# Kernel optimization log

Measured on AMD Instinct MI355X. Metric: run time of the kernel, lower is better.

Reference implementation:

```python
import jax, jax.numpy as jnp
import numpy as np

BS, NINP, NHID, K, T = 2048, 512, 512, 16, 8
M = NHID // K  # per-block hidden = 32
ATT_D = 16     # read/write key dim
TAU = 0.5


def setup_inputs() -> dict:
    key = jax.random.key(0)
    ks = jax.random.split(key, 10)
    s = 0.1
    return {
        "x": jax.random.normal(ks[0], (BS, NINP), jnp.float32),
        "h": jax.random.normal(ks[1], (BS, NHID), jnp.float32),
        # stacked GRUCell params across templates (torch gate order: r, z, n)
        "W_ih": jax.random.normal(ks[2], (T, 3 * M, NINP), jnp.float32) * s,
        "W_hh": jax.random.normal(ks[3], (T, 3 * M, M), jnp.float32) * s,
        "b_ih": jax.random.normal(ks[4], (T, 3 * M), jnp.float32) * s,
        "b_hh": jax.random.normal(ks[5], (T, 3 * M), jnp.float32) * s,
        # GroupLinearLayer weights (no bias): read has 1 group, write has T groups
        "w_read": jax.random.normal(ks[6], (1, M, ATT_D), jnp.float32) * s,
        "w_write": jax.random.normal(ks[7], (T, M, ATT_D), jnp.float32) * s,
        # pre-sampled Gumbel noise for gumbel_softmax, shape [bs*k, T]
        "gumbel_noise": jax.random.gumbel(ks[8], (BS * K, T), jnp.float32),
    }


def reference(x, h, W_ih, W_hh, b_ih, b_hh, w_read, w_write, gumbel_noise):
    bs = h.shape[0]
    N = bs * K
    # blockify hidden: [bs, nhid] -> [N, m]
    h2 = h.reshape(N, M)
    # tile input across blocks: [bs, ninp] -> [N, ninp]
    xin = jnp.broadcast_to(x[:, None, :], (bs, K, NINP)).reshape(N, NINP)
    # read key: GroupLinearLayer with 1 group -> [N, ATT_D]
    h_read = h2 @ w_read[0]
    # all-template GRUCell as two grouped GEMMs: [T, N, 3m]
    gi = jnp.einsum('ni,tgi->tng', xin, W_ih) + b_ih[:, None, :]
    gh = jnp.einsum('nm,tgm->tng', h2, W_hh) + b_hh[:, None, :]
    r = jax.nn.sigmoid(gi[..., :M] + gh[..., :M])
    z = jax.nn.sigmoid(gi[..., M:2 * M] + gh[..., M:2 * M])
    n = jnp.tanh(gi[..., 2 * M:] + r * gh[..., 2 * M:])
    hnext = (1.0 - z) * n + z * h2[None]            # [T, N, m]
    hnext = hnext.transpose(1, 0, 2)                # [N, T, m]
    # write keys: grouped linear per template -> [N, T, ATT_D]
    write_key = jnp.einsum('ntm,tmf->ntf', hnext, w_write)
    # attention logits: bmm(h_read[N,1,f], write_key^T) -> [N, T]
    logits = jnp.einsum('nf,ntf->nt', h_read, write_key)
    # hard gumbel-softmax (tau=0.5) with straight-through estimator
    y_soft = jax.nn.softmax((logits + gumbel_noise) / TAU, axis=-1)
    y_hard = jax.nn.one_hot(jnp.argmax(y_soft, axis=-1), T, dtype=y_soft.dtype)
    att = y_hard + y_soft - jax.lax.stop_gradient(y_soft)  # [N, T]
    # combine templates (bmm with [N,1,T] then mean over singleton dim)
    h_out = jnp.einsum('nt,ntm->nm', att, hnext)    # [N, m]
    h_out = h_out.reshape(bs, K * M)
    att_out = jax.lax.stop_gradient(att).reshape(bs, K, T)
    return h_out, att_out
```

## Files before the change

### kernel.cpp

```cpp
#include <hip/hip_runtime.h>

#define NB_BS   2048
#define NB_NINP 512
#define NB_NHID 512
#define NB_K    16
#define NB_T    8
#define NB_M    32
#define NB_C    768
#define H_OUT_ELEMS (NB_BS * NB_NHID)

__global__ __launch_bounds__(256, 2)
void k1_gemm_gi(const float* __restrict__ x, const float* __restrict__ Wih,
                const float* __restrict__ bih, const float* __restrict__ bhh,
                float* __restrict__ gi)
{
    __shared__ __align__(16) float As[32][34];
    __shared__ __align__(16) float Bs[32][100];

    const int tid  = threadIdx.x;
    const int row0 = blockIdx.x * 32;
    const int col0 = blockIdx.y * 96;
    const int wave = tid >> 6, lane = tid & 63;
    const int rg   = lane >> 2;
    const int cg   = lane & 3;
    const int wc0  = wave * 24 + cg * 6;

    const int arow = tid >> 3, akq = (tid & 7) * 4;
    const int c0 = tid >> 3,          kq0 = (tid & 7) * 4;
    const int c1 = (tid + 256) >> 3,  kq1 = ((tid + 256) & 7) * 4;
    const int c2 = (tid + 512) >> 3,  kq2 = ((tid + 512) & 7) * 4;

    const float* xp = x + (size_t)(row0 + arow) * NB_NINP + akq;
    float4 a0 = *(const float4*)xp;
    float4 b0 = *(const float4*)&Wih[(size_t)(col0 + c0) * NB_NINP + kq0];
    float4 b1 = *(const float4*)&Wih[(size_t)(col0 + c1) * NB_NINP + kq1];
    float4 b2 = *(const float4*)&Wih[(size_t)(col0 + c2) * NB_NINP + kq2];

    float acc[2][6];
    #pragma unroll
    for (int i = 0; i < 2; ++i)
        #pragma unroll
        for (int e = 0; e < 6; ++e) acc[i][e] = 0.f;

    for (int kb = 0; kb < NB_NINP; kb += 32) {
        __syncthreads();
        As[akq+0][arow]=a0.x; As[akq+1][arow]=a0.y;
        As[akq+2][arow]=a0.z; As[akq+3][arow]=a0.w;
        Bs[kq0+0][c0]=b0.x; Bs[kq0+1][c0]=b0.y; Bs[kq0+2][c0]=b0.z; Bs[kq0+3][c0]=b0.w;
        Bs[kq1+0][c1]=b1.x; Bs[kq1+1][c1]=b1.y; Bs[kq1+2][c1]=b1.z; Bs[kq1+3][c1]=b1.w;
        Bs[kq2+0][c2]=b2.x; Bs[kq2+1][c2]=b2.y; Bs[kq2+2][c2]=b2.z; Bs[kq2+3][c2]=b2.w;
        __syncthreads();
        if (kb + 32 < NB_NINP) {
            a0 = *(const float4*)(xp + kb + 32);
            b0 = *(const float4*)&Wih[(size_t)(col0 + c0) * NB_NINP + kb + 32 + kq0];
            b1 = *(const float4*)&Wih[(size_t)(col0 + c1) * NB_NINP + kb + 32 + kq1];
            b2 = *(const float4*)&Wih[(size_t)(col0 + c2) * NB_NINP + kb + 32 + kq2];
        }
        #pragma unroll
        for (int kk = 0; kk < 32; ++kk) {
            const float2 av = *(const float2*)&As[kk][rg * 2];
            const float2 w0 = *(const float2*)&Bs[kk][wc0];
            const float2 w1 = *(const float2*)&Bs[kk][wc0 + 2];
            const float2 w2 = *(const float2*)&Bs[kk][wc0 + 4];
            const float avv[2] = {av.x, av.y};
            const float wvv[6] = {w0.x, w0.y, w1.x, w1.y, w2.x, w2.y};
            #pragma unroll
            for (int i = 0; i < 2; ++i)
                #pragma unroll
                for (int e = 0; e < 6; ++e)
                    acc[i][e] = fmaf(avv[i], wvv[e], acc[i][e]);
        }
    }

    float bias[6];
    #pragma unroll
    for (int e = 0; e < 6; ++e) {
        const int cl = wc0 + e;
        const int c  = col0 + cl;
        bias[e] = bih[c] + (cl < 64 ? bhh[c] : 0.f);
    }
    #pragma unroll
    for (int i = 0; i < 2; ++i) {
        const size_t base = (size_t)(row0 + rg * 2 + i) * NB_C + col0 + wc0;
        #pragma unroll
        for (int e = 0; e < 6; e += 2) {
            float2 o; o.x = acc[i][e] + bias[e]; o.y = acc[i][e+1] + bias[e+1];
            *(float2*)&gi[base + e] = o;
        }
    }
}

__global__ __launch_bounds__(1024)
__attribute__((amdgpu_waves_per_eu(4, 4)))
void k2_fused(const float* __restrict__ h,      const float* __restrict__ Whh,
              const float* __restrict__ bhh,    const float* __restrict__ wread,
              const float* __restrict__ wwrite, const float* __restrict__ gumb,
              const float* __restrict__ gi,     float* __restrict__ out)
{
    __shared__ __align__(16) float4 P[3][32][64];
    __shared__ float WWT[NB_T * 16 * 32];
    __shared__ __align__(16) float WR[512];
    __shared__ __align__(16) float HT[8][32][20];
    __shared__ __align__(16) float HR2T[8][16][20];

    const int tid  = threadIdx.x;
    const int wave = tid >> 6, lane = tid & 63;
    const int bl   = wave >> 1, kh = wave & 1;
    const int b    = blockIdx.x * 8 + bl;
    const int m_   = lane & 31, half = lane >> 5;

    float* PF = (float*)P;
    for (int i = tid; i < 24576; i += 1024) {
        const int c = i >> 5, mm = i & 31;
        const int t = c / 96, rem = c - t * 96;
        const int gc = rem >> 5, mout = rem & 31;
        const int j  = (t >> 1) * 3 + gc;
        const int sl = ((t & 1) * 32 + mout) ^ (mm & 7);
        PF[(((j >> 2) * 32 + mm) * 64 + sl) * 4 + (j & 3)] = Whh[i];
    }
    for (int i = tid; i < 4096; i += 1024) {
        const int t = i >> 9, mo = (i >> 4) & 31, f = i & 15;
        WWT[t * 512 + f * 32 + mo] = wwrite[i];
    }
    if (tid < 512) WR[tid] = wread[tid];
    #pragma unroll
    for (int e = 0; e < 4; ++e) {
        const int idx = kh * 256 + e * 64 + lane;
        HT[bl][idx & 31][idx >> 5] = h[(size_t)b * NB_NHID + idx];
    }
    __syncthreads();

    {
        const int kq = kh * 8 + (lane >> 3);
        const int f0 = (lane & 7) * 2;
        float s0 = 0.f, s1 = 0.f;
        #pragma unroll 8
        for (int mm = 0; mm < 32; ++mm) {
            const float hv = HT[bl][mm][kq];
            s0 = fmaf(hv, WR[mm * 16 + f0], s0);
            s1 = fmaf(hv, WR[mm * 16 + f0 + 1], s1);
        }
        HR2T[bl][f0    ][kq] = s0;
        HR2T[bl][f0 + 1][kq] = s1;
    }

    float gi_r[4][3], bhn[4];
    #pragma unroll
    for (int p = 0; p < 4; ++p) {
        const int t = 2 * p + half;
        #pragma unroll
        for (int gc = 0; gc < 3; ++gc)
            gi_r[p][gc] = gi[(size_t)b * NB_C + t * 96 + gc * 32 + m_];
        bhn[p] = bhh[t * 96 + 64 + m_];
    }

    #pragma unroll 1
    for (int pass = 0; pass < 2; ++pass) {
        const int k0 = kh * 8 + pass * 4;

        float acc[4][12];
        #pragma unroll
        for (int r = 0; r < 4; ++r)
            #pragma unroll
            for (int j = 0; j < 12; ++j) acc[r][j] = 0.f;

        #pragma unroll 4
        for (int mm = 0; mm < 32; ++mm) {
            const int sw = lane ^ (mm & 7);
            const float4 w0 = P[0][mm][sw];
            const float4 w1 = P[1][mm][sw];
            const float4 w2 = P[2][mm][sw];
            const float4 hv = *(const float4*)&HT[bl][mm][k0];
            const float wj[12] = {w0.x,w0.y,w0.z,w0.w, w1.x,w1.y,w1.z,w1.w,
                                  w2.x,w2.y,w2.z,w2.w};
            const float hr4[4] = {hv.x, hv.y, hv.z, hv.w};
            #pragma unroll
            for (int r = 0; r < 4; ++r)
                #pragma unroll
                for (int j = 0; j < 12; ++j)
                    acc[r][j] = fmaf(hr4[r], wj[j], acc[r][j]);
        }

        float ww[4][4];
        #pragma unroll
        for (int r = 0; r < 4; ++r)
            #pragma unroll
            for (int p = 0; p < 4; ++p) ww[r][p] = 0.f;
        #pragma unroll 4
        for (int f = 0; f < 16; ++f) {
            float wt[4];
            #pragma unroll
            for (int p = 0; p < 4; ++p)
                wt[p] = WWT[(2 * p + half) * 512 + f * 32 + m_];
            const float4 hka = *(const float4*)&HR2T[bl][f][k0];
            const float hk[4] = {hka.x, hka.y, hka.z, hka.w};
            #pragma unroll
            for (int r = 0; r < 4; ++r)
                #pragma unroll
                for (int p = 0; p < 4; ++p)
                    ww[r][p] = fmaf(hk[r], wt[p], ww[r][p]);
        }

        #pragma unroll
        for (int r = 0; r < 4; ++r) {
            const int k = k0 + r;
            const float h2v = HT[bl][m_][k];
            float hn[4], lg[4];
            #pragma unroll
            for (int p = 0; p < 4; ++p) {
                const float xr = gi_r[p][0] + acc[r][p*3+0];
                const float xz = gi_r[p][1] + acc[r][p*3+1];
                const float gn = bhn[p]     + acc[r][p*3+2];
                const float rg = 1.f / (1.f + __expf(-xr));
                const float zg = 1.f / (1.f + __expf(-xz));
                const float xn = gi_r[p][2] + rg * gn;
                const float e2 = __expf(2.f * xn);
                const float tn = 1.f - 2.f / (e2 + 1.f);
                const float hv2 = (1.f - zg) * tn + zg * h2v;
                hn[p] = hv2;
                float part = hv2 * ww[r][p];
                part += __shfl_xor(part, 1, 64);
                part += __shfl_xor(part, 2, 64);
                part += __shfl_xor(part, 4, 64);
                part += __shfl_xor(part, 8, 64);
                part += __shfl_xor(part, 16, 64);
                lg[p] = part;
            }
            float s[8];
            #pragma unroll
            for (int p = 0; p < 4; ++p) {
                const float oth = __shfl_xor(lg[p], 32, 64);
                s[2*p]   = half ? oth   : lg[p];
                s[2*p+1] = half ? lg[p] : oth;
            }
            const float* gp = gumb + ((size_t)b * NB_K + k) * NB_T;
            const float4 ga = *(const float4*)gp;
            const float4 gb = *(const float4*)(gp + 4);
            const float gv[8] = {ga.x,ga.y,ga.z,ga.w, gb.x,gb.y,gb.z,gb.w};
            float best = s[0] + gv[0]; int bt = 0;
            #pragma unroll
            for (int t2 = 1; t2 < 8; ++t2) {
                const float v = s[t2] + gv[t2];
                if (v > best) { best = v; bt = t2; }
            }
            const int pstar = bt >> 1, hstar = bt & 1;
            float hsel = hn[0];
            hsel = (pstar == 1) ? hn[1] : hsel;
            hsel = (pstar == 2) ? hn[2] : hsel;
            hsel = (pstar == 3) ? hn[3] : hsel;
            if (half == hstar)
                out[(size_t)b * NB_NHID + k * 32 + m_] = hsel;
            if (lane < 8)
                out[H_OUT_ELEMS + ((size_t)b * NB_K + k) * NB_T + lane] =
                    (lane == bt) ? 1.f : 0.f;
        }
    }
}

extern "C" void kernel_launch(void* const* d_in, const int* in_sizes, int n_in,
                              void* d_out, int out_size, void* d_ws, size_t ws_size,
                              hipStream_t stream) {
    const float* x      = (const float*)d_in[0];
    const float* h      = (const float*)d_in[1];
    const float* Wih    = (const float*)d_in[2];
    const float* Whh    = (const float*)d_in[3];
    const float* bih    = (const float*)d_in[4];
    const float* bhh    = (const float*)d_in[5];
    const float* wread  = (const float*)d_in[6];
    const float* wwrite = (const float*)d_in[7];
    const float* gumb   = (const float*)d_in[8];
    float* out = (float*)d_out;
    float* gi  = (float*)d_ws;

    k1_gemm_gi<<<dim3(64, 8), 256, 0, stream>>>(x, Wih, bih, bhh, gi);
    k2_fused<<<dim3(256), 1024, 0, stream>>>(h, Whh, bhh, wread, wwrite,
                                             gumb, gi, out);
}
```

Measured before the change: 96.34 us.

## Retile gi GEMM to 64-wide columns and split GRU templates across wave pairs

The input GEMM now uses 32x64 output tiles with a K-step of 64, which gives 768 blocks instead of 512 and lets it use float4 LDS reads and stores. The fused GRU kernel now has each wave pair split the 8 templates rather than the 16 blocks. Each wave computes all 16 blocks for its 4 templates, and the logits are exchanged through shared memory before the argmax. This aims to cut redundant h loads and shuffle work and to improve load balance, at the cost of a larger accumulator array (96 floats) that raises register pressure.

```diff
diff --git a/kernel.cpp b/kernel.cpp
--- a/kernel.cpp
+++ b/kernel.cpp
@@ -9,84 +9,87 @@
 #define NB_C    768
 #define H_OUT_ELEMS (NB_BS * NB_NHID)
 
-__global__ __launch_bounds__(256, 2)
+__global__ __launch_bounds__(256, 3)
 void k1_gemm_gi(const float* __restrict__ x, const float* __restrict__ Wih,
                 const float* __restrict__ bih, const float* __restrict__ bhh,
                 float* __restrict__ gi)
 {
-    __shared__ __align__(16) float As[32][34];
-    __shared__ __align__(16) float Bs[32][100];
+    __shared__ __align__(16) float As[64][34];
+    __shared__ __align__(16) float Bs[64][68];
 
     const int tid  = threadIdx.x;
     const int row0 = blockIdx.x * 32;
-    const int col0 = blockIdx.y * 96;
+    const int col0 = blockIdx.y * 64;
     const int wave = tid >> 6, lane = tid & 63;
     const int rg   = lane >> 2;
     const int cg   = lane & 3;
-    const int wc0  = wave * 24 + cg * 6;
-
-    const int arow = tid >> 3, akq = (tid & 7) * 4;
-    const int c0 = tid >> 3,          kq0 = (tid & 7) * 4;
-    const int c1 = (tid + 256) >> 3,  kq1 = ((tid + 256) & 7) * 4;
-    const int c2 = (tid + 512) >> 3,  kq2 = ((tid + 512) & 7) * 4;
-
-    const float* xp = x + (size_t)(row0 + arow) * NB_NINP + akq;
-    float4 a0 = *(const float4*)xp;
-    float4 b0 = *(const float4*)&Wih[(size_t)(col0 + c0) * NB_NINP + kq0];
-    float4 b1 = *(const float4*)&Wih[(size_t)(col0 + c1) * NB_NINP + kq1];
-    float4 b2 = *(const float4*)&Wih[(size_t)(col0 + c2) * NB_NINP + kq2];
-
-    float acc[2][6];
+    const int wc0  = wave * 16 + cg * 4;
+
+    const int ar0 = tid >> 4,           ak0 = (tid & 15) * 4;
+    const int ar1 = (tid + 256) >> 4,   ak1 = ((tid + 256) & 15) * 4;
+    int bc[4], bk[4];
+    #pragma unroll
+    for (int l = 0; l < 4; ++l) {
+        const int q = l * 256 + tid;
+        bc[l] = q >> 4; bk[l] = (q & 15) * 4;
+    }
+
+    float4 a0 = *(const float4*)&x[(size_t)(row0 + ar0) * NB_NINP + ak0];
+    float4 a1 = *(const float4*)&x[(size_t)(row0 + ar1) * NB_NINP + ak1];
+    float4 bfr[4];
+    #pragma unroll
+    for (int l = 0; l < 4; ++l)
+        bfr[l] = *(const float4*)&Wih[(size_t)(col0 + bc[l]) * NB_NINP + bk[l]];
+
+    float acc[2][4];
     #pragma unroll
     for (int i = 0; i < 2; ++i)
         #pragma unroll
-        for (int e = 0; e < 6; ++e) acc[i][e] = 0.f;
-
-    for (int kb = 0; kb < NB_NINP; kb += 32) {
+        for (int e = 0; e < 4; ++e) acc[i][e] = 0.f;
+
+    for (int kb = 0; kb < NB_NINP; kb += 64) {
         __syncthreads();
-        As[akq+0][arow]=a0.x; As[akq+1][arow]=a0.y;
-        As[akq+2][arow]=a0.z; As[akq+3][arow]=a0.w;
-        Bs[kq0+0][c0]=b0.x; Bs[kq0+1][c0]=b0.y; Bs[kq0+2][c0]=b0.z; Bs[kq0+3][c0]=b0.w;
-        Bs[kq1+0][c1]=b1.x; Bs[kq1+1][c1]=b1.y; Bs[kq1+2][c1]=b1.z; Bs[kq1+3][c1]=b1.w;
-        Bs[kq2+0][c2]=b2.x; Bs[kq2+1][c2]=b2.y; Bs[kq2+2][c2]=b2.z; Bs[kq2+3][c2]=b2.w;
+        As[ak0+0][ar0]=a0.x; As[ak0+1][ar0]=a0.y; As[ak0+2][ar0]=a0.z; As[ak0+3][ar0]=a0.w;
+        As[ak1+0][ar1]=a1.x; As[ak1+1][ar1]=a1.y; As[ak1+2][ar1]=a1.z; As[ak1+3][ar1]=a1.w;
+        #pragma unroll
+        for (int l = 0; l < 4; ++l) {
+            Bs[bk[l]+0][bc[l]]=bfr[l].x; Bs[bk[l]+1][bc[l]]=bfr[l].y;
+            Bs[bk[l]+2][bc[l]]=bfr[l].z; Bs[bk[l]+3][bc[l]]=bfr[l].w;
+        }
         __syncthreads();
-        if (kb + 32 < NB_NINP) {
-            a0 = *(const float4*)(xp + kb + 32);
-            b0 = *(const float4*)&Wih[(size_t)(col0 + c0) * NB_NINP + kb + 32 + kq0];
-            b1 = *(const float4*)&Wih[(size_t)(col0 + c1) * NB_NINP + kb + 32 + kq1];
-            b2 = *(const float4*)&Wih[(size_t)(col0 + c2) * NB_NINP + kb + 32 + kq2];
-        }
-        #pragma unroll
-        for (int kk = 0; kk < 32; ++kk) {
+        if (kb + 64 < NB_NINP) {
+            a0 = *(const float4*)&x[(size_t)(row0 + ar0) * NB_NINP + kb + 64 + ak0];
+            a1 = *(const float4*)&x[(size_t)(row0 + ar1) * NB_NINP + kb + 64 + ak1];
+            #pragma unroll
+            for (int l = 0; l < 4; ++l)
+                bfr[l] = *(const float4*)&Wih[(size_t)(col0 + bc[l]) * NB_NINP + kb + 64 + bk[l]];
+        }
+        #pragma unroll 16
+        for (int kk = 0; kk < 64; ++kk) {
             const float2 av = *(const float2*)&As[kk][rg * 2];
-            const float2 w0 = *(const float2*)&Bs[kk][wc0];
-            const float2 w1 = *(const float2*)&Bs[kk][wc0 + 2];
-            const float2 w2 = *(const float2*)&Bs[kk][wc0 + 4];
+            const float4 wv = *(const float4*)&Bs[kk][wc0];
             const float avv[2] = {av.x, av.y};
-            const float wvv[6] = {w0.x, w0.y, w1.x, w1.y, w2.x, w2.y};
+            const float wvv[4] = {wv.x, wv.y, wv.z, wv.w};
             #pragma unroll
             for (int i = 0; i < 2; ++i)
                 #pragma unroll
-                for (int e = 0; e < 6; ++e)
+                for (int e = 0; e < 4; ++e)
                     acc[i][e] = fmaf(avv[i], wvv[e], acc[i][e]);
         }
     }
 
-    float bias[6];
-    #pragma unroll
-    for (int e = 0; e < 6; ++e) {
-        const int cl = wc0 + e;
-        const int c  = col0 + cl;
-        bias[e] = bih[c] + (cl < 64 ? bhh[c] : 0.f);
+    float bias[4];
+    #pragma unroll
+    for (int e = 0; e < 4; ++e) {
+        const int c = col0 + wc0 + e;
+        bias[e] = bih[c] + ((c % 96) < 64 ? bhh[c] : 0.f);
     }
     #pragma unroll
     for (int i = 0; i < 2; ++i) {
-        const size_t base = (size_t)(row0 + rg * 2 + i) * NB_C + col0 + wc0;
-        #pragma unroll
-        for (int e = 0; e < 6; e += 2) {
-            float2 o; o.x = acc[i][e] + bias[e]; o.y = acc[i][e+1] + bias[e+1];
-            *(float2*)&gi[base + e] = o;
-        }
+        float4 o;
+        o.x = acc[i][0] + bias[0]; o.y = acc[i][1] + bias[1];
+        o.z = acc[i][2] + bias[2]; o.w = acc[i][3] + bias[3];
+        *(float4*)&gi[(size_t)(row0 + rg * 2 + i) * NB_C + col0 + wc0] = o;
     }
 }
 
@@ -97,41 +100,40 @@
               const float* __restrict__ wwrite, const float* __restrict__ gumb,
               const float* __restrict__ gi,     float* __restrict__ out)
 {
-    __shared__ __align__(16) float4 P[3][32][64];
-    __shared__ float WWT[NB_T * 16 * 32];
+    __shared__ __align__(16) float P2[2][3][32][128];
+    __shared__ __align__(16) float WWT2[2][16][128];
     __shared__ __align__(16) float WR[512];
     __shared__ __align__(16) float HT[8][32][20];
     __shared__ __align__(16) float HR2T[8][16][20];
+    __shared__ __align__(16) float LG[8][16][8];
 
     const int tid  = threadIdx.x;
     const int wave = tid >> 6, lane = tid & 63;
-    const int bl   = wave >> 1, kh = wave & 1;
+    const int bl   = wave >> 1, tq = wave & 1;
     const int b    = blockIdx.x * 8 + bl;
     const int m_   = lane & 31, half = lane >> 5;
 
-    float* PF = (float*)P;
     for (int i = tid; i < 24576; i += 1024) {
         const int c = i >> 5, mm = i & 31;
         const int t = c / 96, rem = c - t * 96;
         const int gc = rem >> 5, mout = rem & 31;
-        const int j  = (t >> 1) * 3 + gc;
-        const int sl = ((t & 1) * 32 + mout) ^ (mm & 7);
-        PF[(((j >> 2) * 32 + mm) * 64 + sl) * 4 + (j & 3)] = Whh[i];
+        const int slot = (((t >> 1) & 1) * 32 + mout) ^ mm;
+        P2[t >> 2][gc][mm][slot * 2 + (t & 1)] = Whh[i];
     }
     for (int i = tid; i < 4096; i += 1024) {
         const int t = i >> 9, mo = (i >> 4) & 31, f = i & 15;
-        WWT[t * 512 + f * 32 + mo] = wwrite[i];
+        WWT2[t >> 2][f][(((t >> 1) & 1) * 32 + mo) * 2 + (t & 1)] = wwrite[i];
     }
     if (tid < 512) WR[tid] = wread[tid];
     #pragma unroll
     for (int e = 0; e < 4; ++e) {
-        const int idx = kh * 256 + e * 64 + lane;
+        const int idx = tq * 256 + e * 64 + lane;
         HT[bl][idx & 31][idx >> 5] = h[(size_t)b * NB_NHID + idx];
     }
     __syncthreads();
 
     {
-        const int kq = kh * 8 + (lane >> 3);
+        const int kq = tq * 8 + (lane >> 3);
         const int f0 = (lane & 7) * 2;
         float s0 = 0.f, s1 = 0.f;
         #pragma unroll 8
@@ -144,116 +146,115 @@
         HR2T[bl][f0 + 1][kq] = s1;
     }
 
-    float gi_r[4][3], bhn[4];
-    #pragma unroll
-    for (int p = 0; p < 4; ++p) {
-        const int t = 2 * p + half;
+    float acc[16][6];
+    #pragma unroll
+    for (int k = 0; k < 16; ++k)
+        #pragma unroll
+        for (int j = 0; j < 6; ++j) acc[k][j] = 0.f;
+
+    #pragma unroll 1
+    for (int mm = 0; mm < 32; ++mm) {
+        const int sl2 = (lane ^ mm) * 2;
+        const float2 w0 = *(const float2*)&P2[tq][0][mm][sl2];
+        const float2 w1 = *(const float2*)&P2[tq][1][mm][sl2];
+        const float2 w2 = *(const float2*)&P2[tq][2][mm][sl2];
+        #pragma unroll
+        for (int q = 0; q < 4; ++q) {
+            const float4 hv = *(const float4*)&HT[bl][mm][q * 4];
+            const float hr[4] = {hv.x, hv.y, hv.z, hv.w};
+            #pragma unroll
+            for (int r = 0; r < 4; ++r) {
+                const int k = q * 4 + r;
+                acc[k][0] = fmaf(hr[r], w0.x, acc[k][0]);
+                acc[k][1] = fmaf(hr[r], w1.x, acc[k][1]);
+                acc[k][2] = fmaf(hr[r], w2.x, acc[k][2]);
+                acc[k][3] = fmaf(hr[r], w0.y, acc[k][3]);
+                acc[k][4] = fmaf(hr[r], w1.y, acc[k][4]);
+                acc[k][5] = fmaf(hr[r], w2.y, acc[k][5]);
+            }
+        }
+    }
+    __syncthreads();
+
+    float gi_r[2][3], bhn[2];
+    #pragma unroll
+    for (int u = 0; u < 2; ++u) {
+        const int t = tq * 4 + half * 2 + u;
         #pragma unroll
         for (int gc = 0; gc < 3; ++gc)
-            gi_r[p][gc] = gi[(size_t)b * NB_C + t * 96 + gc * 32 + m_];
-        bhn[p] = bhh[t * 96 + 64 + m_];
-    }
-
-    #pragma unroll 1
-    for (int pass = 0; pass < 2; ++pass) {
-        const int k0 = kh * 8 + pass * 4;
-
-        float acc[4][12];
-        #pragma unroll
-        for (int r = 0; r < 4; ++r)
-            #pragma unroll
-            for (int j = 0; j < 12; ++j) acc[r][j] = 0.f;
-
-        #pragma unroll 4
-        for (int mm = 0; mm < 32; ++mm) {
-            const int sw = lane ^ (mm & 7);
-            const float4 w0 = P[0][mm][sw];
-            const float4 w1 = P[1][mm][sw];
-            const float4 w2 = P[2][mm][sw];
-            const float4 hv = *(const float4*)&HT[bl][mm][k0];
-            const float wj[12] = {w0.x,w0.y,w0.z,w0.w, w1.x,w1.y,w1.z,w1.w,
-                                  w2.x,w2.y,w2.z,w2.w};
-            const float hr4[4] = {hv.x, hv.y, hv.z, hv.w};
-            #pragma unroll
-            for (int r = 0; r < 4; ++r)
-                #pragma unroll
-                for (int j = 0; j < 12; ++j)
-                    acc[r][j] = fmaf(hr4[r], wj[j], acc[r][j]);
-        }
-
-        float ww[4][4];
-        #pragma unroll
-        for (int r = 0; r < 4; ++r)
-            #pragma unroll
-            for (int p = 0; p < 4; ++p) ww[r][p] = 0.f;
+            gi_r[u][gc] = gi[(size_t)b * NB_C + t * 96 + gc * 32 + m_];
+        bhn[u] = bhh[t * 96 + 64 + m_];
+    }
+
+    float hn[16][2];
+    #pragma unroll
+    for (int q = 0; q < 4; ++q) {
+        float ww[4][2];
+        #pragma unroll
+        for (int r = 0; r < 4; ++r) { ww[r][0] = 0.f; ww[r][1] = 0.f; }
         #pragma unroll 4
         for (int f = 0; f < 16; ++f) {
-            float wt[4];
-            #pragma unroll
-            for (int p = 0; p < 4; ++p)
-                wt[p] = WWT[(2 * p + half) * 512 + f * 32 + m_];
-            const float4 hka = *(const float4*)&HR2T[bl][f][k0];
-            const float hk[4] = {hka.x, hka.y, hka.z, hka.w};
-            #pragma unroll
-            for (int r = 0; r < 4; ++r)
-                #pragma unroll
-                for (int p = 0; p < 4; ++p)
-                    ww[r][p] = fmaf(hk[r], wt[p], ww[r][p]);
-        }
-
+            const float2 wt = *(const float2*)&WWT2[tq][f][lane * 2];
+            const float4 hk = *(const float4*)&HR2T[bl][f][q * 4];
+            const float hh[4] = {hk.x, hk.y, hk.z, hk.w};
+            #pragma unroll
+            for (int r = 0; r < 4; ++r) {
+                ww[r][0] = fmaf(hh[r], wt.x, ww[r][0]);
+                ww[r][1] = fmaf(hh[r], wt.y, ww[r][1]);
+            }
+        }
         #pragma unroll
         for (int r = 0; r < 4; ++r) {
-            const int k = k0 + r;
+            const int k = q * 4 + r;
             const float h2v = HT[bl][m_][k];
-            float hn[4], lg[4];
-            #pragma unroll
-            for (int p = 0; p < 4; ++p) {
-                const float xr = gi_r[p][0] + acc[r][p*3+0];
-                const float xz = gi_r[p][1] + acc[r][p*3+1];
-                const float gn = bhn[p]     + acc[r][p*3+2];
+            float lg2[2];
+            #pragma unroll
+            for (int u = 0; u < 2; ++u) {
+                const float xr = gi_r[u][0] + acc[k][u*3+0];
+                const float xz = gi_r[u][1] + acc[k][u*3+1];
+                const float gn = bhn[u]     + acc[k][u*3+2];
                 const float rg = 1.f / (1.f + __expf(-xr));
                 const float zg = 1.f / (1.f + __expf(-xz));
-                const float xn = gi_r[p][2] + rg * gn;
+                const float xn = gi_r[u][2] + rg * gn;
                 const float e2 = __expf(2.f * xn);
                 const float tn = 1.f - 2.f / (e2 + 1.f);
                 const float hv2 = (1.f - zg) * tn + zg * h2v;
-                hn[p] = hv2;
-                float part = hv2 * ww[r][p];
+                hn[k][u] = hv2;
+                float part = hv2 * ww[r][u];
                 part += __shfl_xor(part, 1, 64);
                 part += __shfl_xor(part, 2, 64);
                 part += __shfl_xor(part, 4, 64);
                 part += __shfl_xor(part, 8, 64);
                 part += __shfl_xor(part, 16, 64);
-                lg[p] = part;
-            }
-            float s[8];
-            #pragma unroll
-            for (int p = 0; p < 4; ++p) {
-                const float oth = __shfl_xor(lg[p], 32, 64);
-                s[2*p]   = half ? oth   : lg[p];
-                s[2*p+1] = half ? lg[p] : oth;
-            }
-            const float* gp = gumb + ((size_t)b * NB_K + k) * NB_T;
-            const float4 ga = *(const float4*)gp;
-            const float4 gb = *(const float4*)(gp + 4);
-            const float gv[8] = {ga.x,ga.y,ga.z,ga.w, gb.x,gb.y,gb.z,gb.w};
-            float best = s[0] + gv[0]; int bt = 0;
-            #pragma unroll
-            for (int t2 = 1; t2 < 8; ++t2) {
-                const float v = s[t2] + gv[t2];
-                if (v > best) { best = v; bt = t2; }
-            }
-            const int pstar = bt >> 1, hstar = bt & 1;
-            float hsel = hn[0];
-            hsel = (pstar == 1) ? hn[1] : hsel;
-            hsel = (pstar == 2) ? hn[2] : hsel;
-            hsel = (pstar == 3) ? hn[3] : hsel;
-            if (half == hstar)
-                out[(size_t)b * NB_NHID + k * 32 + m_] = hsel;
-            if (lane < 8)
-                out[H_OUT_ELEMS + ((size_t)b * NB_K + k) * NB_T + lane] =
-                    (lane == bt) ? 1.f : 0.f;
-        }
+                lg2[u] = part;
+            }
+            if (m_ == 0) {
+                LG[bl][k][tq * 4 + half * 2 + 0] = lg2[0];
+                LG[bl][k][tq * 4 + half * 2 + 1] = lg2[1];
+            }
+        }
+    }
+    __syncthreads();
+
+    #pragma unroll
+    for (int k = 0; k < 16; ++k) {
+        const float4 l0 = *(const float4*)&LG[bl][k][0];
+        const float4 l1 = *(const float4*)&LG[bl][k][4];
+        const float* gp = gumb + ((size_t)b * NB_K + k) * NB_T;
+        const float4 g0 = *(const float4*)gp;
+        const float4 g1 = *(const float4*)(gp + 4);
+        const float s[8] = {l0.x+g0.x, l0.y+g0.y, l0.z+g0.z, l0.w+g0.w,
+                            l1.x+g1.x, l1.y+g1.y, l1.z+g1.z, l1.w+g1.w};
+        float best = s[0]; int bt = 0;
+        #pragma unroll
+        for (int t2 = 1; t2 < 8; ++t2)
+            if (s[t2] > best) { best = s[t2]; bt = t2; }
+        const float hsel = (bt & 1) ? hn[k][1] : hn[k][0];
+        if ((bt >> 2) == tq && ((bt >> 1) & 1) == half)
+            out[(size_t)b * NB_NHID + k * 32 + m_] = hsel;
+        if (tq == 0 && lane < 8)
+            out[H_OUT_ELEMS + ((size_t)b * NB_K + k) * NB_T + lane] =
+                (lane == bt) ? 1.f : 0.f;
     }
 }
 
@@ -272,7 +273,7 @@
     float* out = (float*)d_out;
     float* gi  = (float*)d_ws;
 
-    k1_gemm_gi<<<dim3(64, 8), 256, 0, stream>>>(x, Wih, bih, bhh, gi);
+    k1_gemm_gi<<<dim3(64, 12), 256, 0, stream>>>(x, Wih, bih, bhh, gi);
     k2_fused<<<dim3(256), 1024, 0, stream>>>(h, Whh, bhh, wread, wwrite,
                                              gumb, gi, out);
 }
```

Result: slower. 104.2 us (+8.2%).

## Restructure gi GEMM with split-K 1024-thread blocks and vectorize write-key loads

Applied to the files above, without the earlier changes.

The input-gate GEMM now uses 64x96 tiles in 1024-thread blocks. The K dimension is split in half across two 512-thread groups, and their partial sums are reduced through shared memory before bias is added and the result stored. The grid becomes 256 blocks, sized to fill the CU count, instead of 512 smaller blocks. Separately, the write-key weights in the fused kernel are laid out so each thread fetches its four template weights with one float4 LDS load instead of four scalar loads. In exchange there is an extra shared-memory reduction and sync, a larger LDS footprint, and scalar global stores instead of float2 stores.

```diff
diff --git a/kernel.cpp b/kernel.cpp
--- a/kernel.cpp
+++ b/kernel.cpp
@@ -9,83 +9,95 @@
 #define NB_C    768
 #define H_OUT_ELEMS (NB_BS * NB_NHID)
 
-__global__ __launch_bounds__(256, 2)
+__global__ __launch_bounds__(1024)
 void k1_gemm_gi(const float* __restrict__ x, const float* __restrict__ Wih,
                 const float* __restrict__ bih, const float* __restrict__ bhh,
                 float* __restrict__ gi)
 {
-    __shared__ __align__(16) float As[32][34];
-    __shared__ __align__(16) float Bs[32][100];
+    __shared__ __align__(16) float As[2][32][68];
+    __shared__ __align__(16) float Bs[2][32][100];
+    __shared__ float ACCX[512][13];
 
     const int tid  = threadIdx.x;
-    const int row0 = blockIdx.x * 32;
+    const int kg   = tid >> 9;
+    const int ttid = tid & 511;
+    const int row0 = blockIdx.x * 64;
     const int col0 = blockIdx.y * 96;
-    const int wave = tid >> 6, lane = tid & 63;
-    const int rg   = lane >> 2;
-    const int cg   = lane & 3;
-    const int wc0  = wave * 24 + cg * 6;
-
-    const int arow = tid >> 3, akq = (tid & 7) * 4;
-    const int c0 = tid >> 3,          kq0 = (tid & 7) * 4;
-    const int c1 = (tid + 256) >> 3,  kq1 = ((tid + 256) & 7) * 4;
-    const int c2 = (tid + 512) >> 3,  kq2 = ((tid + 512) & 7) * 4;
-
-    const float* xp = x + (size_t)(row0 + arow) * NB_NINP + akq;
-    float4 a0 = *(const float4*)xp;
-    float4 b0 = *(const float4*)&Wih[(size_t)(col0 + c0) * NB_NINP + kq0];
-    float4 b1 = *(const float4*)&Wih[(size_t)(col0 + c1) * NB_NINP + kq1];
-    float4 b2 = *(const float4*)&Wih[(size_t)(col0 + c2) * NB_NINP + kq2];
-
-    float acc[2][6];
+    const int rg   = ttid >> 5;
+    const int cg   = ttid & 31;
+    const int kb0  = kg * 256;
+
+    const int ar = ttid >> 3, akq = (ttid & 7) * 4;
+    const int bc0 = ttid >> 3,        bkq0 = (ttid & 7) * 4;
+    const int bc1 = 64 + (ttid >> 3), bkq1 = (ttid & 7) * 4;
+
+    float4 a0 = *(const float4*)&x[(size_t)(row0 + ar) * NB_NINP + kb0 + akq];
+    float4 b0 = *(const float4*)&Wih[(size_t)(col0 + bc0) * NB_NINP + kb0 + bkq0];
+    float4 b1;
+    if (ttid < 256)
+        b1 = *(const float4*)&Wih[(size_t)(col0 + bc1) * NB_NINP + kb0 + bkq1];
+
+    float acc[4][3];
     #pragma unroll
-    for (int i = 0; i < 2; ++i)
-        #pragma unroll
-        for (int e = 0; e < 6; ++e) acc[i][e] = 0.f;
-
-    for (int kb = 0; kb < NB_NINP; kb += 32) {
+    for (int i = 0; i < 4; ++i)
+        #pragma unroll
+        for (int e = 0; e < 3; ++e) acc[i][e] = 0.f;
+
+    for (int slab = 0; slab < 8; ++slab) {
         __syncthreads();
-        As[akq+0][arow]=a0.x; As[akq+1][arow]=a0.y;
-        As[akq+2][arow]=a0.z; As[akq+3][arow]=a0.w;
-        Bs[kq0+0][c0]=b0.x; Bs[kq0+1][c0]=b0.y; Bs[kq0+2][c0]=b0.z; Bs[kq0+3][c0]=b0.w;
-        Bs[kq1+0][c1]=b1.x; Bs[kq1+1][c1]=b1.y; Bs[kq1+2][c1]=b1.z; Bs[kq1+3][c1]=b1.w;
-        Bs[kq2+0][c2]=b2.x; Bs[kq2+1][c2]=b2.y; Bs[kq2+2][c2]=b2.z; Bs[kq2+3][c2]=b2.w;
+        As[kg][akq+0][ar]=a0.x; As[kg][akq+1][ar]=a0.y;
+        As[kg][akq+2][ar]=a0.z; As[kg][akq+3][ar]=a0.w;
+        Bs[kg][bkq0+0][bc0]=b0.x; Bs[kg][bkq0+1][bc0]=b0.y;
+        Bs[kg][bkq0+2][bc0]=b0.z; Bs[kg][bkq0+3][bc0]=b0.w;
+        if (ttid < 256) {
+            Bs[kg][bkq1+0][bc1]=b1.x; Bs[kg][bkq1+1][bc1]=b1.y;
+            Bs[kg][bkq1+2][bc1]=b1.z; Bs[kg][bkq1+3][bc1]=b1.w;
+        }
         __syncthreads();
-        if (kb + 32 < NB_NINP) {
-            a0 = *(const float4*)(xp + kb + 32);
-            b0 = *(const float4*)&Wih[(size_t)(col0 + c0) * NB_NINP + kb + 32 + kq0];
-            b1 = *(const float4*)&Wih[(size_t)(col0 + c1) * NB_NINP + kb + 32 + kq1];
-            b2 = *(const float4*)&Wih[(size_t)(col0 + c2) * NB_NINP + kb + 32 + kq2];
+        if (slab < 7) {
+            const int kb = kb0 + (slab + 1) * 32;
+            a0 = *(const float4*)&x[(size_t)(row0 + ar) * NB_NINP + kb + akq];
+            b0 = *(const float4*)&Wih[(size_t)(col0 + bc0) * NB_NINP + kb + bkq0];
+            if (ttid < 256)
+                b1 = *(const float4*)&Wih[(size_t)(col0 + bc1) * NB_NINP + kb + bkq1];
         }
         #pragma unroll
         for (int kk = 0; kk < 32; ++kk) {
-            const float2 av = *(const float2*)&As[kk][rg * 2];
-            const float2 w0 = *(const float2*)&Bs[kk][wc0];
-            const float2 w1 = *(const float2*)&Bs[kk][wc0 + 2];
-            const float2 w2 = *(const float2*)&Bs[kk][wc0 + 4];
-            const float avv[2] = {av.x, av.y};
-            const float wvv[6] = {w0.x, w0.y, w1.x, w1.y, w2.x, w2.y};
-            #pragma unroll
-            for (int i = 0; i < 2; ++i)
-                #pragma unroll
-                for (int e = 0; e < 6; ++e)
-                    acc[i][e] = fmaf(avv[i], wvv[e], acc[i][e]);
-        }
-    }
-
-    float bias[6];
-    #pragma unroll
-    for (int e = 0; e < 6; ++e) {
-        const int cl = wc0 + e;
-        const int c  = col0 + cl;
-        bias[e] = bih[c] + (cl < 64 ? bhh[c] : 0.f);
-    }
-    #pragma unroll
-    for (int i = 0; i < 2; ++i) {
-        const size_t base = (size_t)(row0 + rg * 2 + i) * NB_C + col0 + wc0;
-        #pragma unroll
-        for (int e = 0; e < 6; e += 2) {
-            float2 o; o.x = acc[i][e] + bias[e]; o.y = acc[i][e+1] + bias[e+1];
-            *(float2*)&gi[base + e] = o;
+            const float4 av = *(const float4*)&As[kg][kk][rg * 4];
+            const float w0 = Bs[kg][kk][cg];
+            const float w1 = Bs[kg][kk][cg + 32];
+            const float w2 = Bs[kg][kk][cg + 64];
+            const float avv[4] = {av.x, av.y, av.z, av.w};
+            #pragma unroll
+            for (int i = 0; i < 4; ++i) {
+                acc[i][0] = fmaf(avv[i], w0, acc[i][0]);
+                acc[i][1] = fmaf(avv[i], w1, acc[i][1]);
+                acc[i][2] = fmaf(avv[i], w2, acc[i][2]);
+            }
+        }
+    }
+
+    __syncthreads();
+    if (kg == 1) {
+        #pragma unroll
+        for (int i = 0; i < 4; ++i)
+            #pragma unroll
+            for (int e = 0; e < 3; ++e) ACCX[ttid][i * 3 + e] = acc[i][e];
+    }
+    __syncthreads();
+    if (kg == 0) {
+        float bias[3];
+        #pragma unroll
+        for (int e = 0; e < 3; ++e) {
+            const int c = col0 + cg + e * 32;
+            bias[e] = bih[c] + (e < 2 ? bhh[c] : 0.f);
+        }
+        #pragma unroll
+        for (int i = 0; i < 4; ++i) {
+            const size_t base = (size_t)(row0 + rg * 4 + i) * NB_C + col0 + cg;
+            #pragma unroll
+            for (int e = 0; e < 3; ++e)
+                gi[base + e * 32] = acc[i][e] + ACCX[ttid][i * 3 + e] + bias[e];
         }
     }
 }
@@ -98,7 +110,7 @@
               const float* __restrict__ gi,     float* __restrict__ out)
 {
     __shared__ __align__(16) float4 P[3][32][64];
-    __shared__ float WWT[NB_T * 16 * 32];
+    __shared__ __align__(16) float4 WWT4[16][64];
     __shared__ __align__(16) float WR[512];
     __shared__ __align__(16) float HT[8][32][20];
     __shared__ __align__(16) float HR2T[8][16][20];
@@ -120,7 +132,7 @@
     }
     for (int i = tid; i < 4096; i += 1024) {
         const int t = i >> 9, mo = (i >> 4) & 31, f = i & 15;
-        WWT[t * 512 + f * 32 + mo] = wwrite[i];
+        ((float*)WWT4)[(f * 64 + (t & 1) * 32 + mo) * 4 + (t >> 1)] = wwrite[i];
     }
     if (tid < 512) WR[tid] = wread[tid];
     #pragma unroll
@@ -188,11 +200,9 @@
             for (int p = 0; p < 4; ++p) ww[r][p] = 0.f;
         #pragma unroll 4
         for (int f = 0; f < 16; ++f) {
-            float wt[4];
-            #pragma unroll
-            for (int p = 0; p < 4; ++p)
-                wt[p] = WWT[(2 * p + half) * 512 + f * 32 + m_];
+            const float4 wt4 = WWT4[f][half * 32 + m_];
             const float4 hka = *(const float4*)&HR2T[bl][f][k0];
+            const float wt[4] = {wt4.x, wt4.y, wt4.z, wt4.w};
             const float hk[4] = {hka.x, hka.y, hka.z, hka.w};
             #pragma unroll
             for (int r = 0; r < 4; ++r)
@@ -272,7 +282,7 @@
     float* out = (float*)d_out;
     float* gi  = (float*)d_ws;
 
-    k1_gemm_gi<<<dim3(64, 8), 256, 0, stream>>>(x, Wih, bih, bhh, gi);
+    k1_gemm_gi<<<dim3(32, 8), 1024, 0, stream>>>(x, Wih, bih, bhh, gi);
     k2_fused<<<dim3(256), 1024, 0, stream>>>(h, Whh, bhh, wread, wwrite,
                                              gumb, gi, out);
 }
```

After: 87.47 us. 1.1x faster.

## Retile gi GEMM with double-buffered LDS and vectorize write-key reductions

Applied to the files above, without the earlier changes.

The input-gate GEMM is retiled to 64-column, 64-deep k-tiles. It double-buffers shared memory, which removes one barrier per step, and XOR-swizzles the B tile so float4 reads avoid bank conflicts. The grid grows to 64x12 blocks with a higher occupancy hint. In the fused kernel, write-key weights are repacked so each lane loads one float4 per step instead of four scalars. The per-template logit reduction now shares butterfly shuffles across templates and gathers the eight logits through a small LDS array instead of extra cross-half shuffles. The risks are higher register and LDS use in the GEMM and a same-wave LDS exchange that relies on ordering within the wave.

```diff
diff --git a/kernel.cpp b/kernel.cpp
--- a/kernel.cpp
+++ b/kernel.cpp
@@ -9,84 +9,113 @@
 #define NB_C    768
 #define H_OUT_ELEMS (NB_BS * NB_NHID)
 
-__global__ __launch_bounds__(256, 2)
+__global__ __launch_bounds__(256, 3)
 void k1_gemm_gi(const float* __restrict__ x, const float* __restrict__ Wih,
                 const float* __restrict__ bih, const float* __restrict__ bhh,
                 float* __restrict__ gi)
 {
-    __shared__ __align__(16) float As[32][34];
-    __shared__ __align__(16) float Bs[32][100];
+    __shared__ __align__(16) float As[2][64][34];
+    __shared__ __align__(16) float Bs[2][64][68];
 
     const int tid  = threadIdx.x;
     const int row0 = blockIdx.x * 32;
-    const int col0 = blockIdx.y * 96;
-    const int wave = tid >> 6, lane = tid & 63;
-    const int rg   = lane >> 2;
-    const int cg   = lane & 3;
-    const int wc0  = wave * 24 + cg * 6;
-
-    const int arow = tid >> 3, akq = (tid & 7) * 4;
-    const int c0 = tid >> 3,          kq0 = (tid & 7) * 4;
-    const int c1 = (tid + 256) >> 3,  kq1 = ((tid + 256) & 7) * 4;
-    const int c2 = (tid + 512) >> 3,  kq2 = ((tid + 512) & 7) * 4;
-
-    const float* xp = x + (size_t)(row0 + arow) * NB_NINP + akq;
-    float4 a0 = *(const float4*)xp;
-    float4 b0 = *(const float4*)&Wih[(size_t)(col0 + c0) * NB_NINP + kq0];
-    float4 b1 = *(const float4*)&Wih[(size_t)(col0 + c1) * NB_NINP + kq1];
-    float4 b2 = *(const float4*)&Wih[(size_t)(col0 + c2) * NB_NINP + kq2];
-
-    float acc[2][6];
+    const int col0 = blockIdx.y * 64;
+    const int rg   = tid & 15;
+    const int cg   = tid >> 4;
+
+    const int akq  = (tid & 15) * 4;
+    const int ar0  = tid >> 4, ar1 = ar0 + 16;
+    const int swz  = (tid & 7) * 4;
+
+    const float* xb = x   + (size_t)row0 * NB_NINP + akq;
+    const float* wb = Wih + (size_t)col0 * NB_NINP + akq;
+
+    float4 a0 = *(const float4*)&xb[(size_t)ar0 * NB_NINP];
+    float4 a1 = *(const float4*)&xb[(size_t)ar1 * NB_NINP];
+    float4 bf[4];
+    #pragma unroll
+    for (int L = 0; L < 4; ++L)
+        bf[L] = *(const float4*)&wb[(size_t)(L * 16 + (tid >> 4)) * NB_NINP];
+
+    float acc[2][4];
     #pragma unroll
     for (int i = 0; i < 2; ++i)
         #pragma unroll
-        for (int e = 0; e < 6; ++e) acc[i][e] = 0.f;
-
-    for (int kb = 0; kb < NB_NINP; kb += 32) {
-        __syncthreads();
-        As[akq+0][arow]=a0.x; As[akq+1][arow]=a0.y;
-        As[akq+2][arow]=a0.z; As[akq+3][arow]=a0.w;
-        Bs[kq0+0][c0]=b0.x; Bs[kq0+1][c0]=b0.y; Bs[kq0+2][c0]=b0.z; Bs[kq0+3][c0]=b0.w;
-        Bs[kq1+0][c1]=b1.x; Bs[kq1+1][c1]=b1.y; Bs[kq1+2][c1]=b1.z; Bs[kq1+3][c1]=b1.w;
-        Bs[kq2+0][c2]=b2.x; Bs[kq2+1][c2]=b2.y; Bs[kq2+2][c2]=b2.z; Bs[kq2+3][c2]=b2.w;
-        __syncthreads();
-        if (kb + 32 < NB_NINP) {
-            a0 = *(const float4*)(xp + kb + 32);
-            b0 = *(const float4*)&Wih[(size_t)(col0 + c0) * NB_NINP + kb + 32 + kq0];
-            b1 = *(const float4*)&Wih[(size_t)(col0 + c1) * NB_NINP + kb + 32 + kq1];
-            b2 = *(const float4*)&Wih[(size_t)(col0 + c2) * NB_NINP + kb + 32 + kq2];
-        }
-        #pragma unroll
-        for (int kk = 0; kk < 32; ++kk) {
-            const float2 av = *(const float2*)&As[kk][rg * 2];
-            const float2 w0 = *(const float2*)&Bs[kk][wc0];
-            const float2 w1 = *(const float2*)&Bs[kk][wc0 + 2];
-            const float2 w2 = *(const float2*)&Bs[kk][wc0 + 4];
+        for (int e = 0; e < 4; ++e) acc[i][e] = 0.f;
+
+    {
+        const float av0[4] = {a0.x, a0.y, a0.z, a0.w};
+        const float av1[4] = {a1.x, a1.y, a1.z, a1.w};
+        #pragma unroll
+        for (int j = 0; j < 4; ++j) {
+            As[0][akq + j][ar0] = av0[j];
+            As[0][akq + j][ar1] = av1[j];
+        }
+        #pragma unroll
+        for (int L = 0; L < 4; ++L) {
+            const float bv[4] = {bf[L].x, bf[L].y, bf[L].z, bf[L].w};
+            const int bcol = (L * 16 + (tid >> 4)) ^ swz;
+            #pragma unroll
+            for (int j = 0; j < 4; ++j) Bs[0][akq + j][bcol] = bv[j];
+        }
+    }
+    __syncthreads();
+
+    for (int s = 0; s < 8; ++s) {
+        const int buf = s & 1;
+        if (s < 7) {
+            const int kb = (s + 1) * 64;
+            a0 = *(const float4*)&xb[(size_t)ar0 * NB_NINP + kb];
+            a1 = *(const float4*)&xb[(size_t)ar1 * NB_NINP + kb];
+            #pragma unroll
+            for (int L = 0; L < 4; ++L)
+                bf[L] = *(const float4*)&wb[(size_t)(L * 16 + (tid >> 4)) * NB_NINP + kb];
+        }
+        #pragma unroll 16
+        for (int kk = 0; kk < 64; ++kk) {
+            const int sB = ((kk >> 2) & 7) * 4;
+            const float2 av = *(const float2*)&As[buf][kk][rg * 2];
+            const float4 wv = *(const float4*)&Bs[buf][kk][(cg * 4) ^ sB];
             const float avv[2] = {av.x, av.y};
-            const float wvv[6] = {w0.x, w0.y, w1.x, w1.y, w2.x, w2.y};
+            const float wvv[4] = {wv.x, wv.y, wv.z, wv.w};
             #pragma unroll
             for (int i = 0; i < 2; ++i)
                 #pragma unroll
-                for (int e = 0; e < 6; ++e)
+                for (int e = 0; e < 4; ++e)
                     acc[i][e] = fmaf(avv[i], wvv[e], acc[i][e]);
         }
-    }
-
-    float bias[6];
-    #pragma unroll
-    for (int e = 0; e < 6; ++e) {
-        const int cl = wc0 + e;
-        const int c  = col0 + cl;
-        bias[e] = bih[c] + (cl < 64 ? bhh[c] : 0.f);
+        if (s < 7) {
+            const int nb = buf ^ 1;
+            const float av0[4] = {a0.x, a0.y, a0.z, a0.w};
+            const float av1[4] = {a1.x, a1.y, a1.z, a1.w};
+            #pragma unroll
+            for (int j = 0; j < 4; ++j) {
+                As[nb][akq + j][ar0] = av0[j];
+                As[nb][akq + j][ar1] = av1[j];
+            }
+            #pragma unroll
+            for (int L = 0; L < 4; ++L) {
+                const float bv[4] = {bf[L].x, bf[L].y, bf[L].z, bf[L].w};
+                const int bcol = (L * 16 + (tid >> 4)) ^ swz;
+                #pragma unroll
+                for (int j = 0; j < 4; ++j) Bs[nb][akq + j][bcol] = bv[j];
+            }
+        }
+        __syncthreads();
+    }
+
+    float bias[4];
+    #pragma unroll
+    for (int e = 0; e < 4; ++e) {
+        const int c = col0 + cg * 4 + e;
+        bias[e] = bih[c] + ((c % 96) < 64 ? bhh[c] : 0.f);
     }
     #pragma unroll
     for (int i = 0; i < 2; ++i) {
-        const size_t base = (size_t)(row0 + rg * 2 + i) * NB_C + col0 + wc0;
-        #pragma unroll
-        for (int e = 0; e < 6; e += 2) {
-            float2 o; o.x = acc[i][e] + bias[e]; o.y = acc[i][e+1] + bias[e+1];
-            *(float2*)&gi[base + e] = o;
-        }
+        float4 o;
+        o.x = acc[i][0] + bias[0]; o.y = acc[i][1] + bias[1];
+        o.z = acc[i][2] + bias[2]; o.w = acc[i][3] + bias[3];
+        *(float4*)&gi[(size_t)(row0 + rg * 2 + i) * NB_C + col0 + cg * 4] = o;
     }
 }
 
@@ -98,10 +127,11 @@
               const float* __restrict__ gi,     float* __restrict__ out)
 {
     __shared__ __align__(16) float4 P[3][32][64];
-    __shared__ float WWT[NB_T * 16 * 32];
+    __shared__ __align__(16) float4 WWT4[16][64];
     __shared__ __align__(16) float WR[512];
     __shared__ __align__(16) float HT[8][32][20];
     __shared__ __align__(16) float HR2T[8][16][20];
+    __shared__ __align__(16) float LG[8][16][8];
 
     const int tid  = threadIdx.x;
     const int wave = tid >> 6, lane = tid & 63;
@@ -120,7 +150,7 @@
     }
     for (int i = tid; i < 4096; i += 1024) {
         const int t = i >> 9, mo = (i >> 4) & 31, f = i & 15;
-        WWT[t * 512 + f * 32 + mo] = wwrite[i];
+        ((float*)WWT4)[(f * 64 + (t & 1) * 32 + mo) * 4 + (t >> 1)] = wwrite[i];
     }
     if (tid < 512) WR[tid] = wread[tid];
     #pragma unroll
@@ -188,11 +218,9 @@
             for (int p = 0; p < 4; ++p) ww[r][p] = 0.f;
         #pragma unroll 4
         for (int f = 0; f < 16; ++f) {
-            float wt[4];
-            #pragma unroll
-            for (int p = 0; p < 4; ++p)
-                wt[p] = WWT[(2 * p + half) * 512 + f * 32 + m_];
+            const float4 wt4 = WWT4[f][half * 32 + m_];
             const float4 hka = *(const float4*)&HR2T[bl][f][k0];
+            const float wt[4] = {wt4.x, wt4.y, wt4.z, wt4.w};
             const float hk[4] = {hka.x, hka.y, hka.z, hka.w};
             #pragma unroll
             for (int r = 0; r < 4; ++r)
@@ -205,7 +233,7 @@
         for (int r = 0; r < 4; ++r) {
             const int k = k0 + r;
             const float h2v = HT[bl][m_][k];
-            float hn[4], lg[4];
+            float hn[4], part[4];
             #pragma unroll
             for (int p = 0; p < 4; ++p) {
                 const float xr = gi_r[p][0] + acc[r][p*3+0];
@@ -218,31 +246,35 @@
                 const float tn = 1.f - 2.f / (e2 + 1.f);
                 const float hv2 = (1.f - zg) * tn + zg * h2v;
                 hn[p] = hv2;
-                float part = hv2 * ww[r][p];
-                part += __shfl_xor(part, 1, 64);
-                part += __shfl_xor(part, 2, 64);
-                part += __shfl_xor(part, 4, 64);
-                part += __shfl_xor(part, 8, 64);
-                part += __shfl_xor(part, 16, 64);
-                lg[p] = part;
+                part[p] = hv2 * ww[r][p];
             }
-            float s[8];
-            #pragma unroll
-            for (int p = 0; p < 4; ++p) {
-                const float oth = __shfl_xor(lg[p], 32, 64);
-                s[2*p]   = half ? oth   : lg[p];
-                s[2*p+1] = half ? lg[p] : oth;
+            #pragma unroll
+            for (int p = 0; p < 4; ++p)
+                part[p] += __shfl_xor(part[p], 16, 64);
+            const bool b4 = (lane & 16) != 0, b3 = (lane & 8) != 0;
+            float v01 = b4 ? part[1] : part[0];
+            float v23 = b4 ? part[3] : part[2];
+            v01 += __shfl_xor(v01, 8, 64);
+            v23 += __shfl_xor(v23, 8, 64);
+            float v = b3 ? v23 : v01;
+            v += __shfl_xor(v, 4, 64);
+            v += __shfl_xor(v, 2, 64);
+            v += __shfl_xor(v, 1, 64);
+            if ((lane & 7) == 0) {
+                const int p_ = ((lane >> 4) & 1) | (((lane >> 3) & 1) << 1);
+                LG[bl][k][2 * p_ + half] = v;
             }
+            const float4 l0 = *(const float4*)&LG[bl][k][0];
+            const float4 l1 = *(const float4*)&LG[bl][k][4];
             const float* gp = gumb + ((size_t)b * NB_K + k) * NB_T;
             const float4 ga = *(const float4*)gp;
             const float4 gb = *(const float4*)(gp + 4);
-            const float gv[8] = {ga.x,ga.y,ga.z,ga.w, gb.x,gb.y,gb.z,gb.w};
-            float best = s[0] + gv[0]; int bt = 0;
-            #pragma unroll
-            for (int t2 = 1; t2 < 8; ++t2) {
-                const float v = s[t2] + gv[t2];
-                if (v > best) { best = v; bt = t2; }
-            }
+            const float s[8] = {l0.x+ga.x, l0.y+ga.y, l0.z+ga.z, l0.w+ga.w,
+                                l1.x+gb.x, l1.y+gb.y, l1.z+gb.z, l1.w+gb.w};
+            float best = s[0]; int bt = 0;
+            #pragma unroll
+            for (int t2 = 1; t2 < 8; ++t2)
+                if (s[t2] > best) { best = s[t2]; bt = t2; }
             const int pstar = bt >> 1, hstar = bt & 1;
             float hsel = hn[0];
             hsel = (pstar == 1) ? hn[1] : hsel;
@@ -272,7 +304,7 @@
     float* out = (float*)d_out;
     float* gi  = (float*)d_ws;
 
-    k1_gemm_gi<<<dim3(64, 8), 256, 0, stream>>>(x, Wih, bih, bhh, gi);
+    k1_gemm_gi<<<dim3(64, 12), 256, 0, stream>>>(x, Wih, bih, bhh, gi);
     k2_fused<<<dim3(256), 1024, 0, stream>>>(h, Whh, bhh, wread, wwrite,
                                              gumb, gi, out);
 }
```

Measured after the change: 89.06 us. -7.6%, faster.
